# Kernel optimization log

Hardware: AMD Instinct MI355X
Metric: run time of the kernel (lower is better)

Reference implementation:

```python
import jax, jax.numpy as jnp
import numpy as np

H = 16
D_MODEL = 1024
D_K = D_MODEL // H  # 64
TEMP = float(np.sqrt(D_K))


def setup_inputs() -> dict:
    key = jax.random.key(0)
    ks = jax.random.split(key, 12)
    N = 2048
    s_in = 1.0 / np.sqrt(D_MODEL)
    inp = {
        "query": jax.random.normal(ks[0], (N, D_MODEL), jnp.float32),
        "key": jax.random.normal(ks[1], (N, D_MODEL), jnp.float32),
        "value": jax.random.normal(ks[2], (N, D_MODEL), jnp.float32),
        "Wq": jax.random.normal(ks[3], (D_MODEL, D_MODEL), jnp.float32) * s_in,
        "bq": jnp.zeros((D_MODEL,), jnp.float32),
        "Wk": jax.random.normal(ks[4], (D_MODEL, D_MODEL), jnp.float32) * s_in,
        "bk": jnp.zeros((D_MODEL,), jnp.float32),
        "Wv": jax.random.normal(ks[5], (D_MODEL, D_MODEL), jnp.float32) * s_in,
        "bv": jnp.zeros((D_MODEL,), jnp.float32),
        "Wo": jax.random.normal(ks[6], (D_MODEL, D_MODEL), jnp.float32) * s_in,
        "bo": jnp.zeros((D_MODEL,), jnp.float32),
    }
    return inp


def reference(query, key, value, Wq, bq, Wk, bk, Wv, bv, Wo, bo):
    # Project then split heads exactly like view(-1, h, d_k).transpose(0, 1):
    # (N, d_model) -> (N, h, d_k) -> (h, N, d_k)
    q = (query @ Wq + bq).reshape(-1, H, D_K).transpose(1, 0, 2)
    k = (key @ Wk + bk).reshape(-1, H, D_K).transpose(1, 0, 2)
    v = (value @ Wv + bv).reshape(-1, H, D_K).transpose(1, 0, 2)
    # Scaled dot-product attention (dropout is inference-mode identity)
    scores = jnp.einsum("hnd,hmd->hnm", q / TEMP, k)  # (h, N, N)
    attn = jax.nn.softmax(scores, axis=-1)
    x = jnp.einsum("hnm,hmd->hnd", attn, v)  # (h, N, d_k)
    x = x.transpose(1, 0, 2).reshape(-1, H * D_K)  # (N, d_model)
    out = x @ Wo + bo
    return (out, attn)
```

## Files before the change

### kernel.cpp

```cpp
#include <hip/hip_runtime.h>
#include <math.h>

#define NTOK 2048
#define DMODEL 1024
#define NHEAD 16
#define DHEAD 64
#define NCH_S 4
#define NCH_A 2
#define TIL_S (NTOK / 64 / NCH_S)
#define TIL_A (NTOK / 64 / NCH_A)

typedef _Float16 f16x8 __attribute__((ext_vector_type(8)));
typedef _Float16 f16x4 __attribute__((ext_vector_type(4)));
typedef _Float16 f16x2 __attribute__((ext_vector_type(2)));
typedef float f32x4 __attribute__((ext_vector_type(4)));
typedef float f32x16 __attribute__((ext_vector_type(16)));

union U32H2 { f16x2 h; unsigned u; };
union U8 { f16x8 v; unsigned u[4]; };

__device__ __forceinline__ void split16(float x, _Float16& hi, _Float16& lo) {
    hi = (_Float16)x;
    lo = (_Float16)(x - (float)hi);
}
__device__ __forceinline__ unsigned packh(_Float16 a, _Float16 b) {
    U32H2 c; c.h = f16x2{a, b}; return c.u;
}

__global__ void __launch_bounds__(256) prep_w_kernel(
        const float* __restrict__ Wq, const float* __restrict__ Wk,
        const float* __restrict__ Wv, const float* __restrict__ Wo,
        _Float16* __restrict__ Wt) {
    __shared__ float T[32][33];
    const int z = blockIdx.z;
    const float* W = (z == 0) ? Wq : (z == 1) ? Wk : (z == 2) ? Wv : Wo;
    _Float16* Whi = Wt + (size_t)z * 2 * 1024 * 1024;
    _Float16* Wlo = Whi + (size_t)1024 * 1024;
    const int t = threadIdx.x;
    const int k0 = blockIdx.y * 32, n0 = blockIdx.x * 32;
    const int r = t >> 3, c4 = (t & 7) * 4;
    const float4 v = *(const float4*)(W + (size_t)(k0 + r) * DMODEL + n0 + c4);
    T[r][c4 + 0] = v.x; T[r][c4 + 1] = v.y; T[r][c4 + 2] = v.z; T[r][c4 + 3] = v.w;
    __syncthreads();
    f16x4 hv, lv;
#pragma unroll
    for (int j = 0; j < 4; ++j) {
        _Float16 h, l;
        split16(T[c4 + j][r], h, l);
        hv[j] = h; lv[j] = l;
    }
    *(f16x4*)(Whi + (size_t)(n0 + r) * DMODEL + k0 + c4) = hv;
    *(f16x4*)(Wlo + (size_t)(n0 + r) * DMODEL + k0 + c4) = lv;
}

__global__ void __launch_bounds__(256) qkv_mfma_kernel(
        const float* __restrict__ Aq, const float* __restrict__ Ak, const float* __restrict__ Av,
        const _Float16* __restrict__ Wt,
        const float* __restrict__ bq, const float* __restrict__ bk, const float* __restrict__ bv,
        _Float16* __restrict__ Qh, _Float16* __restrict__ Ql,
        _Float16* __restrict__ Kh, _Float16* __restrict__ Kl,
        _Float16* __restrict__ Vth, _Float16* __restrict__ Vtl) {
    __shared__ _Float16 Ah[64][40], Al[64][40], Bh[128][40], Bl[128][40];
    const int z = blockIdx.z;
    const float* A = (z == 0) ? Aq : (z == 1) ? Ak : Av;
    const _Float16* WH = Wt + (size_t)z * 2 * 1024 * 1024;
    const _Float16* WL = WH + (size_t)1024 * 1024;
    const float* bias = (z == 0) ? bq : (z == 1) ? bk : bv;

    const int t = threadIdx.x;
    const int l = t & 63, wid = t >> 6;
    const int lr = l & 15, lk = l >> 4;
    const int m0 = blockIdx.y * 64, n0 = blockIdx.x * 128;
    const int wm = (wid >> 1) * 32, wn = (wid & 1) * 64;

    f32x4 acc[2][4];
#pragma unroll
    for (int mi = 0; mi < 2; ++mi)
#pragma unroll
        for (int ni = 0; ni < 4; ++ni)
#pragma unroll
            for (int e = 0; e < 4; ++e) acc[mi][ni][e] = 0.f;

    for (int k0 = 0; k0 < DMODEL; k0 += 32) {
        __syncthreads();
#pragma unroll
        for (int p = 0; p < 2; ++p) {
            const int idx = t + p * 256;
            const int r = idx >> 3, c4 = (idx & 7) * 4;
            const float4 v = *(const float4*)(A + (size_t)(m0 + r) * DMODEL + k0 + c4);
            f16x4 hv, lv; _Float16 h, lo;
            split16(v.x, h, lo); hv[0] = h; lv[0] = lo;
            split16(v.y, h, lo); hv[1] = h; lv[1] = lo;
            split16(v.z, h, lo); hv[2] = h; lv[2] = lo;
            split16(v.w, h, lo); hv[3] = h; lv[3] = lo;
            *(f16x4*)&Ah[r][c4] = hv;
            *(f16x4*)&Al[r][c4] = lv;
        }
#pragma unroll
        for (int p = 0; p < 2; ++p) {
            const int idx = t + p * 256;
            const int r = idx >> 2, c8 = (idx & 3) * 8;
            *(f16x8*)&Bh[r][c8] = *(const f16x8*)(WH + (size_t)(n0 + r) * DMODEL + k0 + c8);
            *(f16x8*)&Bl[r][c8] = *(const f16x8*)(WL + (size_t)(n0 + r) * DMODEL + k0 + c8);
        }
        __syncthreads();

        f16x8 ah[2], al[2], bh[4], bl[4];
#pragma unroll
        for (int i = 0; i < 2; ++i) {
            ah[i] = *(f16x8*)&Ah[wm + i * 16 + lr][lk * 8];
            al[i] = *(f16x8*)&Al[wm + i * 16 + lr][lk * 8];
        }
#pragma unroll
        for (int i = 0; i < 4; ++i) {
            bh[i] = *(f16x8*)&Bh[wn + i * 16 + lr][lk * 8];
            bl[i] = *(f16x8*)&Bl[wn + i * 16 + lr][lk * 8];
        }
#pragma unroll
        for (int mi = 0; mi < 2; ++mi)
#pragma unroll
            for (int ni = 0; ni < 4; ++ni) {
                acc[mi][ni] = __builtin_amdgcn_mfma_f32_16x16x32_f16(ah[mi], bh[ni], acc[mi][ni], 0, 0, 0);
                acc[mi][ni] = __builtin_amdgcn_mfma_f32_16x16x32_f16(ah[mi], bl[ni], acc[mi][ni], 0, 0, 0);
                acc[mi][ni] = __builtin_amdgcn_mfma_f32_16x16x32_f16(al[mi], bh[ni], acc[mi][ni], 0, 0, 0);
            }
    }

#pragma unroll
    for (int ni = 0; ni < 4; ++ni) {
        const int col = n0 + wn + ni * 16 + lr;
        const float bv_ = bias[col];
#pragma unroll
        for (int mi = 0; mi < 2; ++mi) {
            if (z == 2) {
                f16x4 hv, lv;
#pragma unroll
                for (int i = 0; i < 4; ++i) {
                    _Float16 h, lo;
                    split16(acc[mi][ni][i] + bv_, h, lo);
                    hv[i] = h; lv[i] = lo;
                }
                const int row = m0 + wm + mi * 16 + lk * 4;
                *(f16x4*)(Vth + (size_t)col * NTOK + row) = hv;
                *(f16x4*)(Vtl + (size_t)col * NTOK + row) = lv;
            } else {
#pragma unroll
                for (int i = 0; i < 4; ++i) {
                    const int row = m0 + wm + mi * 16 + lk * 4 + i;
                    float v = acc[mi][ni][i] + bv_;
                    if (z == 0) v *= 0.125f;
                    _Float16 h, lo;
                    split16(v, h, lo);
                    if (z == 0) { Qh[(size_t)row * DMODEL + col] = h; Ql[(size_t)row * DMODEL + col] = lo; }
                    else        { Kh[(size_t)row * DMODEL + col] = h; Kl[(size_t)row * DMODEL + col] = lo; }
                }
            }
        }
    }
}

__global__ void __launch_bounds__(256, 4) stats_kernel(
        const _Float16* __restrict__ Qh, const _Float16* __restrict__ Ql,
        const _Float16* __restrict__ Kh, const _Float16* __restrict__ Kl,
        float* __restrict__ lpart) {
    __shared__ _Float16 KB[2][2][64][64];
    const int t = threadIdx.x, l = t & 63, w = t >> 6, q = l & 31, h = l >> 5;
    const int hh = blockIdx.y, z = blockIdx.z;
    const int rw = blockIdx.x * 128 + w * 32;
    const int sr = t >> 3, sc = t & 7;

    f16x8 qbh[4], qbl[4];
#pragma unroll
    for (int s = 0; s < 4; ++s) {
        const size_t off = (size_t)(rw + q) * DMODEL + hh * DHEAD + s * 16 + h * 8;
        qbh[s] = *(const f16x8*)(Qh + off);
        qbl[s] = *(const f16x8*)(Ql + off);
    }

    float lsum = 0.f;
    {
        const int j0 = z * TIL_S * 64;
#pragma unroll
        for (int p = 0; p < 2; ++p) {
            const int r = sr + p * 32; const int cs = (sc ^ (r & 7)) * 8;
            *(f16x8*)&KB[0][0][r][cs] = *(const f16x8*)(Kh + (size_t)(j0 + r) * DMODEL + hh * DHEAD + sc * 8);
            *(f16x8*)&KB[0][1][r][cs] = *(const f16x8*)(Kl + (size_t)(j0 + r) * DMODEL + hh * DHEAD + sc * 8);
        }
    }
    for (int it = 0; it < TIL_S; ++it) {
        __syncthreads();
        const int cur = it & 1;
        if (it + 1 < TIL_S) {
            const int j0 = (z * TIL_S + it + 1) * 64;
#pragma unroll
            for (int p = 0; p < 2; ++p) {
                const int r = sr + p * 32; const int cs = (sc ^ (r & 7)) * 8;
                *(f16x8*)&KB[cur ^ 1][0][r][cs] = *(const f16x8*)(Kh + (size_t)(j0 + r) * DMODEL + hh * DHEAD + sc * 8);
                *(f16x8*)&KB[cur ^ 1][1][r][cs] = *(const f16x8*)(Kl + (size_t)(j0 + r) * DMODEL + hh * DHEAD + sc * 8);
            }
        }
#pragma unroll
        for (int kb = 0; kb < 2; ++kb) {
            f32x16 c;
#pragma unroll
            for (int r = 0; r < 16; ++r) c[r] = 0.f;
            __builtin_amdgcn_s_setprio(1);
#pragma unroll
            for (int s = 0; s < 4; ++s) {
                const int rk = kb * 32 + q; const int cc = ((2 * s + h) ^ (rk & 7)) * 8;
                const f16x8 ah = *(f16x8*)&KB[cur][0][rk][cc];
                const f16x8 al = *(f16x8*)&KB[cur][1][rk][cc];
                c = __builtin_amdgcn_mfma_f32_32x32x16_f16(ah, qbh[s], c, 0, 0, 0);
                c = __builtin_amdgcn_mfma_f32_32x32x16_f16(ah, qbl[s], c, 0, 0, 0);
                c = __builtin_amdgcn_mfma_f32_32x32x16_f16(al, qbh[s], c, 0, 0, 0);
            }
            __builtin_amdgcn_s_setprio(0);
#pragma unroll
            for (int r = 0; r < 16; ++r) lsum += __expf(c[r]);
        }
    }
    lsum += __shfl_xor(lsum, 32);
    if (h == 0) lpart[((size_t)z * NHEAD + hh) * NTOK + rw + q] = lsum;
}

__global__ void __launch_bounds__(256, 2) attnpv_kernel(
        const _Float16* __restrict__ Qh, const _Float16* __restrict__ Ql,
        const _Float16* __restrict__ Kh, const _Float16* __restrict__ Kl,
        const _Float16* __restrict__ Vth, const _Float16* __restrict__ Vtl,
        const float* __restrict__ lpart,
        float* __restrict__ attn, float* __restrict__ Xp0, float* __restrict__ Xp1) {
    __shared__ _Float16 KB[2][2][64][64];
    __shared__ _Float16 VB[2][2][64][64];
    const int t = threadIdx.x, l = t & 63, w = t >> 6, q = l & 31, h = l >> 5;
    const int hh = blockIdx.y, z = blockIdx.z;
    const int rw = blockIdx.x * 128 + w * 32;
    const int sr = t >> 3, sc = t & 7;
    const int qrow = rw + q;

    float lsum = 0.f;
#pragma unroll
    for (int zz = 0; zz < NCH_S; ++zz) lsum += lpart[((size_t)zz * NHEAD + hh) * NTOK + qrow];
    const float linv = 1.f / lsum;

    f16x8 qbh[4], qbl[4];
#pragma unroll
    for (int s = 0; s < 4; ++s) {
        const size_t off = (size_t)qrow * DMODEL + hh * DHEAD + s * 16 + h * 8;
        qbh[s] = *(const f16x8*)(Qh + off);
        qbl[s] = *(const f16x8*)(Ql + off);
    }

    f32x16 x0, x1;
#pragma unroll
    for (int r = 0; r < 16; ++r) { x0[r] = 0.f; x1[r] = 0.f; }

    auto stage = [&](int buf, int j0) {
#pragma unroll
        for (int p = 0; p < 2; ++p) {
            const int r = sr + p * 32; const int cs = (sc ^ (r & 7)) * 8;
            *(f16x8*)&KB[buf][0][r][cs] = *(const f16x8*)(Kh + (size_t)(j0 + r) * DMODEL + hh * DHEAD + sc * 8);
            *(f16x8*)&KB[buf][1][r][cs] = *(const f16x8*)(Kl + (size_t)(j0 + r) * DMODEL + hh * DHEAD + sc * 8);
            *(f16x8*)&VB[buf][0][r][cs] = *(const f16x8*)(Vth + (size_t)(hh * DHEAD + r) * NTOK + j0 + sc * 8);
            *(f16x8*)&VB[buf][1][r][cs] = *(const f16x8*)(Vtl + (size_t)(hh * DHEAD + r) * NTOK + j0 + sc * 8);
        }
    };
    stage(0, z * TIL_A * 64);

    for (int it = 0; it < TIL_A; ++it) {
        const int j0 = (z * TIL_A + it) * 64;
        __syncthreads();
        const int cur = it & 1;
        if (it + 1 < TIL_A) stage(cur ^ 1, (z * TIL_A + it + 1) * 64);

#pragma unroll
        for (int kb = 0; kb < 2; ++kb) {
            f32x16 c;
#pragma unroll
            for (int r = 0; r < 16; ++r) c[r] = 0.f;
            __builtin_amdgcn_s_setprio(1);
#pragma unroll
            for (int s = 0; s < 4; ++s) {
                const int rk = kb * 32 + q; const int cc = ((2 * s + h) ^ (rk & 7)) * 8;
                const f16x8 ah = *(f16x8*)&KB[cur][0][rk][cc];
                const f16x8 al = *(f16x8*)&KB[cur][1][rk][cc];
                c = __builtin_amdgcn_mfma_f32_32x32x16_f16(ah, qbh[s], c, 0, 0, 0);
                c = __builtin_amdgcn_mfma_f32_32x32x16_f16(ah, qbl[s], c, 0, 0, 0);
                c = __builtin_amdgcn_mfma_f32_32x32x16_f16(al, qbh[s], c, 0, 0, 0);
            }
            __builtin_amdgcn_s_setprio(0);

            float p[16];
#pragma unroll
            for (int r = 0; r < 16; ++r) p[r] = __expf(c[r]) * linv;

            const int kbase = j0 + kb * 32;
#pragma unroll
            for (int i = 0; i < 4; ++i) {
                const float4 st = make_float4(p[4 * i], p[4 * i + 1], p[4 * i + 2], p[4 * i + 3]);
                *(float4*)(attn + ((size_t)hh * NTOK + qrow) * NTOK + kbase + 8 * i + 4 * h) = st;
            }

            _Float16 hf[16], lf[16];
#pragma unroll
            for (int r = 0; r < 16; ++r) {
                hf[r] = (_Float16)p[r];
                lf[r] = (_Float16)(p[r] - (float)hf[r]);
            }
            unsigned ph[8], pl[8];
#pragma unroll
            for (int i = 0; i < 8; ++i) {
                ph[i] = packh(hf[2 * i], hf[2 * i + 1]);
                pl[i] = packh(lf[2 * i], lf[2 * i + 1]);
            }

#pragma unroll
            for (int ss = 0; ss < 2; ++ss) {
                const int b = 4 * ss;
                const unsigned eh0 = __shfl_xor(h ? ph[b + 0] : ph[b + 2], 32);
                const unsigned eh1 = __shfl_xor(h ? ph[b + 1] : ph[b + 3], 32);
                const unsigned el0 = __shfl_xor(h ? pl[b + 0] : pl[b + 2], 32);
                const unsigned el1 = __shfl_xor(h ? pl[b + 1] : pl[b + 3], 32);
                U8 pah, pal;
                pah.u[0] = h ? eh0 : ph[b + 0]; pah.u[1] = h ? eh1 : ph[b + 1];
                pah.u[2] = h ? ph[b + 2] : eh0; pah.u[3] = h ? ph[b + 3] : eh1;
                pal.u[0] = h ? el0 : pl[b + 0]; pal.u[1] = h ? el1 : pl[b + 1];
                pal.u[2] = h ? pl[b + 2] : el0; pal.u[3] = h ? pl[b + 3] : el1;
                const int ks = kb * 2 + ss;
                __builtin_amdgcn_s_setprio(1);
                {
                    const int rd0 = q; const int cv0 = ((2 * ks + h) ^ (rd0 & 7)) * 8;
                    const f16x8 vh = *(f16x8*)&VB[cur][0][rd0][cv0];
                    const f16x8 vl = *(f16x8*)&VB[cur][1][rd0][cv0];
                    x0 = __builtin_amdgcn_mfma_f32_32x32x16_f16(pah.v, vh, x0, 0, 0, 0);
                    x0 = __builtin_amdgcn_mfma_f32_32x32x16_f16(pah.v, vl, x0, 0, 0, 0);
                    x0 = __builtin_amdgcn_mfma_f32_32x32x16_f16(pal.v, vh, x0, 0, 0, 0);
                }
                {
                    const int rd1 = 32 + q; const int cv1 = ((2 * ks + h) ^ (rd1 & 7)) * 8;
                    const f16x8 vh = *(f16x8*)&VB[cur][0][rd1][cv1];
                    const f16x8 vl = *(f16x8*)&VB[cur][1][rd1][cv1];
                    x1 = __builtin_amdgcn_mfma_f32_32x32x16_f16(pah.v, vh, x1, 0, 0, 0);
                    x1 = __builtin_amdgcn_mfma_f32_32x32x16_f16(pah.v, vl, x1, 0, 0, 0);
                    x1 = __builtin_amdgcn_mfma_f32_32x32x16_f16(pal.v, vh, x1, 0, 0, 0);
                }
                __builtin_amdgcn_s_setprio(0);
            }
        }
    }

    float* __restrict__ Xout = z ? Xp1 : Xp0;
#pragma unroll
    for (int r = 0; r < 16; ++r) {
        const int qloc = (r & 3) + 8 * (r >> 2) + 4 * h;
        Xout[(size_t)(rw + qloc) * DMODEL + hh * DHEAD + q]      = x0[r];
        Xout[(size_t)(rw + qloc) * DMODEL + hh * DHEAD + 32 + q] = x1[r];
    }
}

__global__ void __launch_bounds__(256) out_mfma_kernel(
        const float* __restrict__ Xp0, const float* __restrict__ Xp1,
        const _Float16* __restrict__ WH, const _Float16* __restrict__ WL,
        const float* __restrict__ bo, float* __restrict__ out) {
    __shared__ _Float16 Ah[64][40], Al[64][40], Bh[128][40], Bl[128][40];
    const int t = threadIdx.x;
    const int l = t & 63, wid = t >> 6;
    const int lr = l & 15, lk = l >> 4;
    const int m0 = blockIdx.y * 64, n0 = blockIdx.x * 128;
    const int wm = (wid >> 1) * 32, wn = (wid & 1) * 64;

    f32x4 acc[2][4];
#pragma unroll
    for (int mi = 0; mi < 2; ++mi)
#pragma unroll
        for (int ni = 0; ni < 4; ++ni)
#pragma unroll
            for (int e = 0; e < 4; ++e) acc[mi][ni][e] = 0.f;

    for (int k0 = 0; k0 < DMODEL; k0 += 32) {
        __syncthreads();
#pragma unroll
        for (int p = 0; p < 2; ++p) {
            const int idx = t + p * 256;
            const int r = idx >> 3, c4 = (idx & 7) * 4;
            const size_t off = (size_t)(m0 + r) * DMODEL + k0 + c4;
            const float4 v0 = *(const float4*)(Xp0 + off);
            const float4 v1 = *(const float4*)(Xp1 + off);
            f16x4 hv, lv; _Float16 h, lo;
            split16(v0.x + v1.x, h, lo); hv[0] = h; lv[0] = lo;
            split16(v0.y + v1.y, h, lo); hv[1] = h; lv[1] = lo;
            split16(v0.z + v1.z, h, lo); hv[2] = h; lv[2] = lo;
            split16(v0.w + v1.w, h, lo); hv[3] = h; lv[3] = lo;
            *(f16x4*)&Ah[r][c4] = hv;
            *(f16x4*)&Al[r][c4] = lv;
        }
#pragma unroll
        for (int p = 0; p < 2; ++p) {
            const int idx = t + p * 256;
            const int r = idx >> 2, c8 = (idx & 3) * 8;
            *(f16x8*)&Bh[r][c8] = *(const f16x8*)(WH + (size_t)(n0 + r) * DMODEL + k0 + c8);
            *(f16x8*)&Bl[r][c8] = *(const f16x8*)(WL + (size_t)(n0 + r) * DMODEL + k0 + c8);
        }
        __syncthreads();

        f16x8 ah[2], al[2], bh[4], bl[4];
#pragma unroll
        for (int i = 0; i < 2; ++i) {
            ah[i] = *(f16x8*)&Ah[wm + i * 16 + lr][lk * 8];
            al[i] = *(f16x8*)&Al[wm + i * 16 + lr][lk * 8];
        }
#pragma unroll
        for (int i = 0; i < 4; ++i) {
            bh[i] = *(f16x8*)&Bh[wn + i * 16 + lr][lk * 8];
            bl[i] = *(f16x8*)&Bl[wn + i * 16 + lr][lk * 8];
        }
#pragma unroll
        for (int mi = 0; mi < 2; ++mi)
#pragma unroll
            for (int ni = 0; ni < 4; ++ni) {
                acc[mi][ni] = __builtin_amdgcn_mfma_f32_16x16x32_f16(ah[mi], bh[ni], acc[mi][ni], 0, 0, 0);
                acc[mi][ni] = __builtin_amdgcn_mfma_f32_16x16x32_f16(ah[mi], bl[ni], acc[mi][ni], 0, 0, 0);
                acc[mi][ni] = __builtin_amdgcn_mfma_f32_16x16x32_f16(al[mi], bh[ni], acc[mi][ni], 0, 0, 0);
            }
    }

#pragma unroll
    for (int ni = 0; ni < 4; ++ni) {
        const int col = n0 + wn + ni * 16 + lr;
        const float bv_ = bo[col];
#pragma unroll
        for (int mi = 0; mi < 2; ++mi)
#pragma unroll
            for (int i = 0; i < 4; ++i) {
                const int row = m0 + wm + mi * 16 + lk * 4 + i;
                out[(size_t)row * DMODEL + col] = acc[mi][ni][i] + bv_;
            }
    }
}

extern "C" void kernel_launch(void* const* d_in, const int* in_sizes, int n_in,
                              void* d_out, int out_size, void* d_ws, size_t ws_size,
                              hipStream_t stream) {
    (void)in_sizes; (void)n_in; (void)out_size; (void)ws_size;
    const float* query = (const float*)d_in[0];
    const float* key_  = (const float*)d_in[1];
    const float* value = (const float*)d_in[2];
    const float* Wq = (const float*)d_in[3];
    const float* bq = (const float*)d_in[4];
    const float* Wk = (const float*)d_in[5];
    const float* bk = (const float*)d_in[6];
    const float* Wv = (const float*)d_in[7];
    const float* bv = (const float*)d_in[8];
    const float* Wo = (const float*)d_in[9];
    const float* bo = (const float*)d_in[10];

    float* out  = (float*)d_out;
    float* attn = out + (size_t)NTOK * DMODEL;

    const size_t MM = (size_t)1024 * 1024;
    _Float16* ws16 = (_Float16*)d_ws;
    _Float16* Wt  = ws16;
    _Float16* Qh  = ws16 + 8 * MM;
    _Float16* Ql  = Qh  + 2 * MM;
    _Float16* Kh_ = Ql  + 2 * MM;
    _Float16* Kl_ = Kh_ + 2 * MM;
    _Float16* Vth = Kl_ + 2 * MM;
    _Float16* Vtl = Vth + 2 * MM;

    float* Xp0   = (float*)ws16;
    float* lpart = (float*)(ws16 + 4 * MM);
    float* Xp1   = (float*)(ws16 + 20 * MM);

    dim3 blk(256);
    prep_w_kernel<<<dim3(32, 32, 4), blk, 0, stream>>>(Wq, Wk, Wv, Wo, Wt);
    qkv_mfma_kernel<<<dim3(8, 32, 3), blk, 0, stream>>>(query, key_, value, Wt, bq, bk, bv,
                                                        Qh, Ql, Kh_, Kl_, Vth, Vtl);
    stats_kernel<<<dim3(16, 16, NCH_S), blk, 0, stream>>>(Qh, Ql, Kh_, Kl_, lpart);
    attnpv_kernel<<<dim3(16, 16, NCH_A), blk, 0, stream>>>(Qh, Ql, Kh_, Kl_, Vth, Vtl,
                                                           lpart, attn, Xp0, Xp1);
    out_mfma_kernel<<<dim3(8, 32), blk, 0, stream>>>(Xp0, Xp1, Wt + 6 * MM, Wt + 7 * MM, bo, out);
}
```

Before: 243.0 us.

## Pre-split activations to fp16 hi/lo and enlarge GEMM M tiles to 128

A new prep kernel converts query/key/value into fp16 hi/lo planes once, staged in the attn output buffer. The QKV GEMM then loads them directly instead of splitting per tile. Both projection GEMMs move from 64x128 to 128x128 tiles with a 4x4 MFMA accumulator per wave, raising reuse of the loaded B tiles. Both also raise wave priority around the MFMA block. In exchange there is an extra kernel pass over the activations, fewer blocks in the grid (possible underfill of CUs), and higher register/LDS use.

```diff
diff --git a/kernel.cpp b/kernel.cpp
--- a/kernel.cpp
+++ b/kernel.cpp
@@ -53,16 +53,42 @@
     *(f16x4*)(Wlo + (size_t)(n0 + r) * DMODEL + k0 + c4) = lv;
 }
 
+__global__ void __launch_bounds__(256) prep_a_kernel(
+        const float* __restrict__ q, const float* __restrict__ k, const float* __restrict__ v,
+        _Float16* __restrict__ As) {
+    const int z = blockIdx.y;
+    const float* A = (z == 0) ? q : (z == 1) ? k : v;
+    const size_t PL = (size_t)NTOK * DMODEL;
+    _Float16* H = As + (size_t)z * 2 * PL;
+    _Float16* L = H + PL;
+    const size_t off = ((size_t)blockIdx.x * 256 + threadIdx.x) * 8;
+    const float4 a = *(const float4*)(A + off);
+    const float4 b = *(const float4*)(A + off + 4);
+    f16x8 hv, lv; _Float16 h, lo;
+    split16(a.x, h, lo); hv[0] = h; lv[0] = lo;
+    split16(a.y, h, lo); hv[1] = h; lv[1] = lo;
+    split16(a.z, h, lo); hv[2] = h; lv[2] = lo;
+    split16(a.w, h, lo); hv[3] = h; lv[3] = lo;
+    split16(b.x, h, lo); hv[4] = h; lv[4] = lo;
+    split16(b.y, h, lo); hv[5] = h; lv[5] = lo;
+    split16(b.z, h, lo); hv[6] = h; lv[6] = lo;
+    split16(b.w, h, lo); hv[7] = h; lv[7] = lo;
+    *(f16x8*)(H + off) = hv;
+    *(f16x8*)(L + off) = lv;
+}
+
 __global__ void __launch_bounds__(256) qkv_mfma_kernel(
-        const float* __restrict__ Aq, const float* __restrict__ Ak, const float* __restrict__ Av,
+        const _Float16* __restrict__ As,
         const _Float16* __restrict__ Wt,
         const float* __restrict__ bq, const float* __restrict__ bk, const float* __restrict__ bv,
         _Float16* __restrict__ Qh, _Float16* __restrict__ Ql,
         _Float16* __restrict__ Kh, _Float16* __restrict__ Kl,
         _Float16* __restrict__ Vth, _Float16* __restrict__ Vtl) {
-    __shared__ _Float16 Ah[64][40], Al[64][40], Bh[128][40], Bl[128][40];
+    __shared__ _Float16 Ah[128][40], Al[128][40], Bh[128][40], Bl[128][40];
     const int z = blockIdx.z;
-    const float* A = (z == 0) ? Aq : (z == 1) ? Ak : Av;
+    const size_t PL = (size_t)NTOK * DMODEL;
+    const _Float16* AH = As + (size_t)z * 2 * PL;
+    const _Float16* AL = AH + PL;
     const _Float16* WH = Wt + (size_t)z * 2 * 1024 * 1024;
     const _Float16* WL = WH + (size_t)1024 * 1024;
     const float* bias = (z == 0) ? bq : (z == 1) ? bk : bv;
@@ -70,12 +96,12 @@
     const int t = threadIdx.x;
     const int l = t & 63, wid = t >> 6;
     const int lr = l & 15, lk = l >> 4;
-    const int m0 = blockIdx.y * 64, n0 = blockIdx.x * 128;
-    const int wm = (wid >> 1) * 32, wn = (wid & 1) * 64;
-
-    f32x4 acc[2][4];
-#pragma unroll
-    for (int mi = 0; mi < 2; ++mi)
+    const int m0 = blockIdx.y * 128, n0 = blockIdx.x * 128;
+    const int wm = (wid >> 1) * 64, wn = (wid & 1) * 64;
+
+    f32x4 acc[4][4];
+#pragma unroll
+    for (int mi = 0; mi < 4; ++mi)
 #pragma unroll
         for (int ni = 0; ni < 4; ++ni)
 #pragma unroll
@@ -83,47 +109,35 @@
 
     for (int k0 = 0; k0 < DMODEL; k0 += 32) {
         __syncthreads();
-#pragma unroll
-        for (int p = 0; p < 2; ++p) {
-            const int idx = t + p * 256;
-            const int r = idx >> 3, c4 = (idx & 7) * 4;
-            const float4 v = *(const float4*)(A + (size_t)(m0 + r) * DMODEL + k0 + c4);
-            f16x4 hv, lv; _Float16 h, lo;
-            split16(v.x, h, lo); hv[0] = h; lv[0] = lo;
-            split16(v.y, h, lo); hv[1] = h; lv[1] = lo;
-            split16(v.z, h, lo); hv[2] = h; lv[2] = lo;
-            split16(v.w, h, lo); hv[3] = h; lv[3] = lo;
-            *(f16x4*)&Ah[r][c4] = hv;
-            *(f16x4*)&Al[r][c4] = lv;
-        }
 #pragma unroll
         for (int p = 0; p < 2; ++p) {
             const int idx = t + p * 256;
             const int r = idx >> 2, c8 = (idx & 3) * 8;
+            *(f16x8*)&Ah[r][c8] = *(const f16x8*)(AH + (size_t)(m0 + r) * DMODEL + k0 + c8);
+            *(f16x8*)&Al[r][c8] = *(const f16x8*)(AL + (size_t)(m0 + r) * DMODEL + k0 + c8);
             *(f16x8*)&Bh[r][c8] = *(const f16x8*)(WH + (size_t)(n0 + r) * DMODEL + k0 + c8);
             *(f16x8*)&Bl[r][c8] = *(const f16x8*)(WL + (size_t)(n0 + r) * DMODEL + k0 + c8);
         }
         __syncthreads();
 
-        f16x8 ah[2], al[2], bh[4], bl[4];
-#pragma unroll
-        for (int i = 0; i < 2; ++i) {
+        f16x8 ah[4], al[4], bh[4], bl[4];
+#pragma unroll
+        for (int i = 0; i < 4; ++i) {
             ah[i] = *(f16x8*)&Ah[wm + i * 16 + lr][lk * 8];
             al[i] = *(f16x8*)&Al[wm + i * 16 + lr][lk * 8];
-        }
-#pragma unroll
-        for (int i = 0; i < 4; ++i) {
             bh[i] = *(f16x8*)&Bh[wn + i * 16 + lr][lk * 8];
             bl[i] = *(f16x8*)&Bl[wn + i * 16 + lr][lk * 8];
         }
-#pragma unroll
-        for (int mi = 0; mi < 2; ++mi)
+        __builtin_amdgcn_s_setprio(1);
+#pragma unroll
+        for (int mi = 0; mi < 4; ++mi)
 #pragma unroll
             for (int ni = 0; ni < 4; ++ni) {
                 acc[mi][ni] = __builtin_amdgcn_mfma_f32_16x16x32_f16(ah[mi], bh[ni], acc[mi][ni], 0, 0, 0);
                 acc[mi][ni] = __builtin_amdgcn_mfma_f32_16x16x32_f16(ah[mi], bl[ni], acc[mi][ni], 0, 0, 0);
                 acc[mi][ni] = __builtin_amdgcn_mfma_f32_16x16x32_f16(al[mi], bh[ni], acc[mi][ni], 0, 0, 0);
             }
+        __builtin_amdgcn_s_setprio(0);
     }
 
 #pragma unroll
@@ -131,7 +145,7 @@
         const int col = n0 + wn + ni * 16 + lr;
         const float bv_ = bias[col];
 #pragma unroll
-        for (int mi = 0; mi < 2; ++mi) {
+        for (int mi = 0; mi < 4; ++mi) {
             if (z == 2) {
                 f16x4 hv, lv;
 #pragma unroll
@@ -361,16 +375,16 @@
         const float* __restrict__ Xp0, const float* __restrict__ Xp1,
         const _Float16* __restrict__ WH, const _Float16* __restrict__ WL,
         const float* __restrict__ bo, float* __restrict__ out) {
-    __shared__ _Float16 Ah[64][40], Al[64][40], Bh[128][40], Bl[128][40];
+    __shared__ _Float16 Ah[128][40], Al[128][40], Bh[128][40], Bl[128][40];
     const int t = threadIdx.x;
     const int l = t & 63, wid = t >> 6;
     const int lr = l & 15, lk = l >> 4;
-    const int m0 = blockIdx.y * 64, n0 = blockIdx.x * 128;
-    const int wm = (wid >> 1) * 32, wn = (wid & 1) * 64;
-
-    f32x4 acc[2][4];
-#pragma unroll
-    for (int mi = 0; mi < 2; ++mi)
+    const int m0 = blockIdx.y * 128, n0 = blockIdx.x * 128;
+    const int wm = (wid >> 1) * 64, wn = (wid & 1) * 64;
+
+    f32x4 acc[4][4];
+#pragma unroll
+    for (int mi = 0; mi < 4; ++mi)
 #pragma unroll
         for (int ni = 0; ni < 4; ++ni)
 #pragma unroll
@@ -379,7 +393,7 @@
     for (int k0 = 0; k0 < DMODEL; k0 += 32) {
         __syncthreads();
 #pragma unroll
-        for (int p = 0; p < 2; ++p) {
+        for (int p = 0; p < 4; ++p) {
             const int idx = t + p * 256;
             const int r = idx >> 3, c4 = (idx & 7) * 4;
             const size_t off = (size_t)(m0 + r) * DMODEL + k0 + c4;
@@ -402,25 +416,24 @@
         }
         __syncthreads();
 
-        f16x8 ah[2], al[2], bh[4], bl[4];
-#pragma unroll
-        for (int i = 0; i < 2; ++i) {
+        f16x8 ah[4], al[4], bh[4], bl[4];
+#pragma unroll
+        for (int i = 0; i < 4; ++i) {
             ah[i] = *(f16x8*)&Ah[wm + i * 16 + lr][lk * 8];
             al[i] = *(f16x8*)&Al[wm + i * 16 + lr][lk * 8];
-        }
-#pragma unroll
-        for (int i = 0; i < 4; ++i) {
             bh[i] = *(f16x8*)&Bh[wn + i * 16 + lr][lk * 8];
             bl[i] = *(f16x8*)&Bl[wn + i * 16 + lr][lk * 8];
         }
-#pragma unroll
-        for (int mi = 0; mi < 2; ++mi)
+        __builtin_amdgcn_s_setprio(1);
+#pragma unroll
+        for (int mi = 0; mi < 4; ++mi)
 #pragma unroll
             for (int ni = 0; ni < 4; ++ni) {
                 acc[mi][ni] = __builtin_amdgcn_mfma_f32_16x16x32_f16(ah[mi], bh[ni], acc[mi][ni], 0, 0, 0);
                 acc[mi][ni] = __builtin_amdgcn_mfma_f32_16x16x32_f16(ah[mi], bl[ni], acc[mi][ni], 0, 0, 0);
                 acc[mi][ni] = __builtin_amdgcn_mfma_f32_16x16x32_f16(al[mi], bh[ni], acc[mi][ni], 0, 0, 0);
             }
+        __builtin_amdgcn_s_setprio(0);
     }
 
 #pragma unroll
@@ -428,7 +441,7 @@
         const int col = n0 + wn + ni * 16 + lr;
         const float bv_ = bo[col];
 #pragma unroll
-        for (int mi = 0; mi < 2; ++mi)
+        for (int mi = 0; mi < 4; ++mi)
 #pragma unroll
             for (int i = 0; i < 4; ++i) {
                 const int row = m0 + wm + mi * 16 + lk * 4 + i;
@@ -470,12 +483,15 @@
     float* lpart = (float*)(ws16 + 4 * MM);
     float* Xp1   = (float*)(ws16 + 20 * MM);
 
+    _Float16* As = (_Float16*)attn;
+
     dim3 blk(256);
     prep_w_kernel<<<dim3(32, 32, 4), blk, 0, stream>>>(Wq, Wk, Wv, Wo, Wt);
-    qkv_mfma_kernel<<<dim3(8, 32, 3), blk, 0, stream>>>(query, key_, value, Wt, bq, bk, bv,
+    prep_a_kernel<<<dim3(1024, 3), blk, 0, stream>>>(query, key_, value, As);
+    qkv_mfma_kernel<<<dim3(8, 16, 3), blk, 0, stream>>>(As, Wt, bq, bk, bv,
                                                         Qh, Ql, Kh_, Kl_, Vth, Vtl);
     stats_kernel<<<dim3(16, 16, NCH_S), blk, 0, stream>>>(Qh, Ql, Kh_, Kl_, lpart);
     attnpv_kernel<<<dim3(16, 16, NCH_A), blk, 0, stream>>>(Qh, Ql, Kh_, Kl_, Vth, Vtl,
                                                            lpart, attn, Xp0, Xp1);
-    out_mfma_kernel<<<dim3(8, 32), blk, 0, stream>>>(Xp0, Xp1, Wt + 6 * MM, Wt + 7 * MM, bo, out);
-}
+    out_mfma_kernel<<<dim3(8, 16), blk, 0, stream>>>(Xp0, Xp1, Wt + 6 * MM, Wt + 7 * MM, bo, out);
+}
```

Result: slower. 276.0 us (+13.6%).
